# Performance work log

Hardware: AMD Instinct MI355X
Metric: run time of the kernel (lower is better)

Reference implementation:

```python
import jax, jax.numpy as jnp
import numpy as np
import math

B, S, D, H = 2, 2048, 1024, 16
HD = D // H  # 64 head dim
DFF = 4 * D
ROPE_BASE = 10000.0
EPS = 1e-5


def setup_inputs() -> dict:
    key = jax.random.key(0)
    ks = jax.random.split(key, 16)
    w = lambda k, shp: jax.random.normal(k, shp, jnp.float32) * 0.02
    return {
        "x": jax.random.normal(ks[0], (B, S, D), jnp.float32),
        "Wq": w(ks[1], (D, D)), "bq": jnp.zeros((D,), jnp.float32),
        "Wk": w(ks[2], (D, D)), "bk": jnp.zeros((D,), jnp.float32),
        "Wv": w(ks[3], (D, D)), "bv": jnp.zeros((D,), jnp.float32),
        "Wo": w(ks[4], (D, D)), "bo": jnp.zeros((D,), jnp.float32),
        "W1": w(ks[5], (D, DFF)), "b1": jnp.zeros((DFF,), jnp.float32),
        "W2": w(ks[6], (DFF, D)), "b2": jnp.zeros((D,), jnp.float32),
        "g_pre": jnp.ones((D,), jnp.float32), "be_pre": jnp.zeros((D,), jnp.float32),
        "g_post": jnp.ones((D,), jnp.float32), "be_post": jnp.zeros((D,), jnp.float32),
    }


def _layernorm(x, g, b):
    mu = jnp.mean(x, axis=-1, keepdims=True)
    var = jnp.mean(jnp.square(x - mu), axis=-1, keepdims=True)
    return (x - mu) * jax.lax.rsqrt(var + EPS) * g + b


def _rope(q, k):
    # q,k: [B,H,S,HD]; standard rotary embedding on head dim
    half = HD // 2
    inv_freq = 1.0 / (ROPE_BASE ** (jnp.arange(0, HD, 2, dtype=jnp.float32) / HD))  # [half]
    pos = jnp.arange(S, dtype=jnp.float32)
    freqs = pos[:, None] * inv_freq[None, :]           # [S, half]
    emb = jnp.concatenate([freqs, freqs], axis=-1)      # [S, HD]
    cos = jnp.cos(emb)[None, None]                      # [1,1,S,HD]
    sin = jnp.sin(emb)[None, None]

    def rot_half(t):
        return jnp.concatenate([-t[..., half:], t[..., :half]], axis=-1)

    return q * cos + rot_half(q) * sin, k * cos + rot_half(k) * sin


def reference(x, Wq, bq, Wk, bk, Wv, bv, Wo, bo, W1, b1, W2, b2,
              g_pre, be_pre, g_post, be_post):
    residual = x
    xn = _layernorm(x, g_pre, be_pre)

    def split_heads(t):  # [B,S,D] -> [B,H,S,HD]
        return t.reshape(B, S, H, HD).transpose(0, 2, 1, 3)

    q = split_heads(xn @ Wq + bq)
    k = split_heads(xn @ Wk + bk)
    v = split_heads(xn @ Wv + bv)
    q, k = _rope(q, k)

    scores = jnp.einsum("bhqd,bhkd->bhqk", q, k) / math.sqrt(HD)
    attn = jax.nn.softmax(scores, axis=-1)
    # NOTE: original applies causal mask AFTER softmax with fill -1e9 (no renorm)
    causal = jnp.tril(jnp.ones((S, S), jnp.float32))
    attn = jnp.where(causal == 0, jnp.float32(-1e9), attn)

    out = jnp.einsum("bhqk,bhkd->bhqd", attn, v)        # [B,H,S,HD]
    out = out.transpose(0, 2, 1, 3).reshape(B, S, D)
    out = out @ Wo + bo
    x = residual + out

    residual = x
    xn = _layernorm(x, g_post, be_post)
    ff = jax.nn.relu(xn @ W1 + b1) @ W2 + b2
    return residual + ff
```

## Files before the change

kernel.cpp:

```cpp
#include <hip/hip_runtime.h>
#include <stdint.h>

#define B_ 2
#define S_ 2048
#define D_ 1024
#define H_ 16
#define HD_ 64
#define DFF_ 4096
#define M_ 4096
#define QKV_STR 3072

typedef float           f4_t  __attribute__((ext_vector_type(4)));
typedef unsigned int    ui4_t __attribute__((ext_vector_type(4)));
typedef unsigned int    ui2_t __attribute__((ext_vector_type(2)));
typedef unsigned short  us4_t __attribute__((ext_vector_type(4)));
typedef unsigned short  us8_t __attribute__((ext_vector_type(8)));
typedef __bf16          bf8_t __attribute__((ext_vector_type(8)));

__device__ __forceinline__ float b2f(unsigned short u) {
    union { unsigned int u; float f; } v; v.u = ((unsigned int)u) << 16; return v.f;
}
__device__ __forceinline__ unsigned short f2b(float f) {
    union { float f; unsigned int u; } v; v.f = f;
    unsigned int u = v.u + 0x7fffu + ((v.u >> 16) & 1u);
    return (unsigned short)(u >> 16);
}
__device__ __forceinline__ unsigned cvt_pk_bf16(float lo, float hi) {
    unsigned r;
    asm("v_cvt_pk_bf16_f32 %0, %1, %2" : "=v"(r) : "v"(lo), "v"(hi));
    return r;
}
__device__ __forceinline__ void gll16(const unsigned short* g, unsigned short* l) {
    __builtin_amdgcn_global_load_lds((const __attribute__((address_space(1))) unsigned int*)g,
                                     (__attribute__((address_space(3))) unsigned int*)l,
                                     16, 0, 0);
}

__global__ __launch_bounds__(256) void k_transpose(const float* __restrict__ in,
                                                   unsigned short* __restrict__ out,
                                                   int R, int C) {
    __shared__ float tile[32][33];
    const int bc = blockIdx.x * 32, br = blockIdx.y * 32;
    const int tx = threadIdx.x & 31, ty = threadIdx.x >> 5;
#pragma unroll
    for (int i = ty; i < 32; i += 8)
        tile[i][tx] = in[(size_t)(br + i) * C + bc + tx];
    __syncthreads();
#pragma unroll
    for (int i = ty; i < 32; i += 8)
        out[(size_t)(bc + i) * R + br + tx] = f2b(tile[tx][i]);
}

__global__ __launch_bounds__(256) void k_bias3(const float* __restrict__ a,
                                               const float* __restrict__ b,
                                               const float* __restrict__ c,
                                               float* __restrict__ o) {
    const int t = blockIdx.x * 256 + threadIdx.x;
    if (t < 1024) o[t] = a[t];
    else if (t < 2048) o[t] = b[t - 1024];
    else o[t] = c[t - 2048];
}

__global__ __launch_bounds__(256) void k_layernorm(const float* __restrict__ x,
                                                   const float* __restrict__ g,
                                                   const float* __restrict__ be,
                                                   unsigned short* __restrict__ out) {
    const int row = blockIdx.x;
    const int t = threadIdx.x;
    const float* xr = x + (size_t)row * D_;
    f4_t v = *(const f4_t*)&xr[t * 4];
    float s = v[0] + v[1] + v[2] + v[3];
#pragma unroll
    for (int o = 32; o >= 1; o >>= 1) s += __shfl_down(s, o);
    __shared__ float red[4];
    const int w = t >> 6, lane = t & 63;
    if (lane == 0) red[w] = s;
    __syncthreads();
    const float mean = (red[0] + red[1] + red[2] + red[3]) * (1.f / D_);
    f4_t d;
#pragma unroll
    for (int c = 0; c < 4; c++) d[c] = v[c] - mean;
    float ss = d[0]*d[0] + d[1]*d[1] + d[2]*d[2] + d[3]*d[3];
#pragma unroll
    for (int o = 32; o >= 1; o >>= 1) ss += __shfl_down(ss, o);
    __syncthreads();
    if (lane == 0) red[w] = ss;
    __syncthreads();
    const float var = (red[0] + red[1] + red[2] + red[3]) * (1.f / D_);
    const float rstd = rsqrtf(var + 1e-5f);
    f4_t gv = *(const f4_t*)&g[t * 4];
    f4_t bv = *(const f4_t*)&be[t * 4];
    us4_t o4;
#pragma unroll
    for (int c = 0; c < 4; c++) o4[c] = f2b(d[c] * rstd * gv[c] + bv[c]);
    *(us4_t*)&out[(size_t)row * D_ + t * 4] = o4;
}

template<int RELU, int BF16OUT, int RESID>
__global__ __launch_bounds__(256) void k_gemm_bt(const unsigned short* __restrict__ A,
                                                 const unsigned short* __restrict__ Bt,
                                                 const float* __restrict__ bias,
                                                 const float* __restrict__ resid,
                                                 void* __restrict__ Cout,
                                                 int M, int N, int K) {
    __shared__ __align__(16) unsigned short As0[128 * 32];
    __shared__ __align__(16) unsigned short Bs0[128 * 32];
    __shared__ __align__(16) unsigned short As1[128 * 32];
    __shared__ __align__(16) unsigned short Bs1[128 * 32];
    const int tid = threadIdx.x;
    const int m0 = blockIdx.y * 128, n0 = blockIdx.x * 128;
    const int w = tid >> 6, lane = tid & 63;
    const int wr = w >> 1, wc = w & 1;
    const int lr = lane & 15, lg = lane >> 4;

    f4_t acc[4][4] = {};

    const int r1 = tid >> 2, q1 = tid & 3;
    const unsigned short* pA1 = A + (size_t)(m0 + r1) * K + q1 * 8;
    const unsigned short* pA2 = pA1 + (size_t)64 * K;
    const unsigned short* pB1 = Bt + (size_t)(n0 + r1) * K + q1 * 8;
    const unsigned short* pB2 = pB1 + (size_t)64 * K;
    const int wofs = w * 512;

#define STAGE(AS, BS, kk) do {                 \
        gll16(pA1 + (kk), (AS) + wofs);        \
        gll16(pA2 + (kk), (AS) + 2048 + wofs); \
        gll16(pB1 + (kk), (BS) + wofs);        \
        gll16(pB2 + (kk), (BS) + 2048 + wofs); } while (0)

#define COMPUTE(AS, BS) do {                                                     \
        bf8_t af[4], bfr[4];                                                     \
        _Pragma("unroll")                                                        \
        for (int f = 0; f < 4; f++) {                                            \
            af[f]  = *(const bf8_t*)&(AS)[(wr * 64 + f * 16 + lr) * 32 + lg * 8];\
            bfr[f] = *(const bf8_t*)&(BS)[(wc * 64 + f * 16 + lr) * 32 + lg * 8];\
        }                                                                        \
        _Pragma("unroll")                                                        \
        for (int mf = 0; mf < 4; mf++)                                           \
            _Pragma("unroll")                                                    \
            for (int nf = 0; nf < 4; nf++)                                       \
                acc[mf][nf] = __builtin_amdgcn_mfma_f32_16x16x32_bf16(           \
                    af[mf], bfr[nf], acc[mf][nf], 0, 0, 0); } while (0)

    STAGE(As0, Bs0, 0);
    for (int k0 = 0; k0 + 64 < K; k0 += 64) {
        STAGE(As1, Bs1, k0 + 32);
        asm volatile("s_waitcnt vmcnt(4)" ::: "memory");
        __builtin_amdgcn_s_barrier();
        COMPUTE(As0, Bs0);
        __builtin_amdgcn_s_barrier();
        STAGE(As0, Bs0, k0 + 64);
        asm volatile("s_waitcnt vmcnt(4)" ::: "memory");
        __builtin_amdgcn_s_barrier();
        COMPUTE(As1, Bs1);
        __builtin_amdgcn_s_barrier();
    }
    STAGE(As1, Bs1, K - 32);
    asm volatile("s_waitcnt vmcnt(4)" ::: "memory");
    __builtin_amdgcn_s_barrier();
    COMPUTE(As0, Bs0);
    asm volatile("s_waitcnt vmcnt(0)" ::: "memory");
    __builtin_amdgcn_s_barrier();
    COMPUTE(As1, Bs1);
#undef STAGE
#undef COMPUTE

#pragma unroll
    for (int mf = 0; mf < 4; mf++) {
#pragma unroll
        for (int nf = 0; nf < 4; nf++) {
            const int n = n0 + wc * 64 + nf * 16 + lr;
            const float bv = bias[n];
#pragma unroll
            for (int j = 0; j < 4; j++) {
                const int m = m0 + wr * 64 + mf * 16 + lg * 4 + j;
                float val = acc[mf][nf][j] + bv;
                if (RESID) val += resid[(size_t)m * N + n];
                if (RELU) val = fmaxf(val, 0.f);
                if (BF16OUT) ((unsigned short*)Cout)[(size_t)m * N + n] = f2b(val);
                else         ((float*)Cout)[(size_t)m * N + n] = val;
            }
        }
    }
}

template<int RELU, int BF16OUT, int RESID>
__global__ __launch_bounds__(256) void k_gemm64(const unsigned short* __restrict__ A,
                                                const unsigned short* __restrict__ Bt,
                                                const float* __restrict__ bias,
                                                const float* __restrict__ resid,
                                                void* __restrict__ Cout,
                                                int M, int N, int K) {
    __shared__ __align__(16) unsigned short As0[64 * 32];
    __shared__ __align__(16) unsigned short Bs0[128 * 32];
    __shared__ __align__(16) unsigned short As1[64 * 32];
    __shared__ __align__(16) unsigned short Bs1[128 * 32];
    const int tid = threadIdx.x;
    const int m0 = blockIdx.y * 64, n0 = blockIdx.x * 128;
    const int w = tid >> 6, lane = tid & 63;
    const int wr = w >> 1, wc = w & 1;
    const int lr = lane & 15, lg = lane >> 4;

    f4_t acc[2][4] = {};

    const int r1 = tid >> 2, q1 = tid & 3;
    const unsigned short* pA1 = A + (size_t)(m0 + r1) * K + q1 * 8;
    const unsigned short* pB1 = Bt + (size_t)(n0 + r1) * K + q1 * 8;
    const unsigned short* pB2 = pB1 + (size_t)64 * K;
    const int wofs = w * 512;

#define STAGE(AS, BS, kk) do {                 \
        gll16(pA1 + (kk), (AS) + wofs);        \
        gll16(pB1 + (kk), (BS) + wofs);        \
        gll16(pB2 + (kk), (BS) + 2048 + wofs); } while (0)

#define COMPUTE(AS, BS) do {                                                     \
        bf8_t af[2], bfr[4];                                                     \
        _Pragma("unroll")                                                        \
        for (int f = 0; f < 2; f++)                                              \
            af[f] = *(const bf8_t*)&(AS)[(wr * 32 + f * 16 + lr) * 32 + lg * 8]; \
        _Pragma("unroll")                                                        \
        for (int f = 0; f < 4; f++)                                              \
            bfr[f] = *(const bf8_t*)&(BS)[(wc * 64 + f * 16 + lr) * 32 + lg * 8];\
        _Pragma("unroll")                                                        \
        for (int mf = 0; mf < 2; mf++)                                           \
            _Pragma("unroll")                                                    \
            for (int nf = 0; nf < 4; nf++)                                       \
                acc[mf][nf] = __builtin_amdgcn_mfma_f32_16x16x32_bf16(           \
                    af[mf], bfr[nf], acc[mf][nf], 0, 0, 0); } while (0)

    STAGE(As0, Bs0, 0);
    for (int k0 = 0; k0 + 64 < K; k0 += 64) {
        STAGE(As1, Bs1, k0 + 32);
        asm volatile("s_waitcnt vmcnt(3)" ::: "memory");
        __builtin_amdgcn_s_barrier();
        COMPUTE(As0, Bs0);
        __builtin_amdgcn_s_barrier();
        STAGE(As0, Bs0, k0 + 64);
        asm volatile("s_waitcnt vmcnt(3)" ::: "memory");
        __builtin_amdgcn_s_barrier();
        COMPUTE(As1, Bs1);
        __builtin_amdgcn_s_barrier();
    }
    STAGE(As1, Bs1, K - 32);
    asm volatile("s_waitcnt vmcnt(3)" ::: "memory");
    __builtin_amdgcn_s_barrier();
    COMPUTE(As0, Bs0);
    asm volatile("s_waitcnt vmcnt(0)" ::: "memory");
    __builtin_amdgcn_s_barrier();
    COMPUTE(As1, Bs1);
#undef STAGE
#undef COMPUTE

#pragma unroll
    for (int mf = 0; mf < 2; mf++) {
#pragma unroll
        for (int nf = 0; nf < 4; nf++) {
            const int n = n0 + wc * 64 + nf * 16 + lr;
            const float bv = bias[n];
#pragma unroll
            for (int j = 0; j < 4; j++) {
                const int m = m0 + wr * 32 + mf * 16 + lg * 4 + j;
                float val = acc[mf][nf][j] + bv;
                if (RESID) val += resid[(size_t)m * N + n];
                if (RELU) val = fmaxf(val, 0.f);
                if (BF16OUT) ((unsigned short*)Cout)[(size_t)m * N + n] = f2b(val);
                else         ((float*)Cout)[(size_t)m * N + n] = val;
            }
        }
    }
}

__global__ __launch_bounds__(256) void k_rope(unsigned short* __restrict__ QKV) {
    const int idx = blockIdx.x * 256 + threadIdx.x;
    const int i = idx & 31;
    const int h = (idx >> 5) & 15;
    const int s = (idx >> 9) & 2047;
    const int b = idx >> 20;
    const float freq = exp2f(-(float)i * 0.4152410118609203f);
    const float ang = (float)s * freq;
    float sn, cs;
    sincosf(ang, &sn, &cs);
    const size_t base = ((size_t)(b * S_ + s)) * QKV_STR + h * HD_ + i;
    {
        float a = b2f(QKV[base]), c2 = b2f(QKV[base + 32]);
        QKV[base]      = f2b(a * cs - c2 * sn);
        QKV[base + 32] = f2b(c2 * cs + a * sn);
    }
    {
        float a = b2f(QKV[base + 1024]), c2 = b2f(QKV[base + 1024 + 32]);
        QKV[base + 1024]      = f2b(a * cs - c2 * sn);
        QKV[base + 1024 + 32] = f2b(c2 * cs + a * sn);
    }
}

__global__ __launch_bounds__(256) void k_vchunksum(const unsigned short* __restrict__ V,
                                                   float* __restrict__ sums) {
    const int blk = blockIdx.x;
    const int bh = blk >> 5, c = blk & 31;
    const int b = bh >> 4, h = bh & 15;
    const int d = threadIdx.x & 63, r4 = threadIdx.x >> 6;
    const unsigned short* base = V + ((size_t)(b * S_ + c * 64 + r4 * 16)) * QKV_STR + h * HD_ + d;
    float s = 0.f;
#pragma unroll
    for (int r = 0; r < 16; r++) s += b2f(base[(size_t)r * QKV_STR]);
    __shared__ float red[4][64];
    red[r4][d] = s;
    __syncthreads();
    if (r4 == 0) sums[(size_t)blk * 64 + d] = red[0][d] + red[1][d] + red[2][d] + red[3][d];
}

__global__ __launch_bounds__(64) void k_vscan(const float* __restrict__ sums,
                                              float* __restrict__ pre) {
    const int bh = blockIdx.x, d = threadIdx.x;
    float cum = 0.f;
    for (int c = 0; c < 32; c++) {
        pre[((size_t)bh * 33 + c) * 64 + d] = cum;
        cum += sums[((size_t)bh * 32 + c) * 64 + d];
    }
    pre[((size_t)bh * 33 + 32) * 64 + d] = cum;
}

#define KS_STRIDE 72

__global__ __launch_bounds__(256) void k_attn_mfma(const unsigned short* __restrict__ QKV,
                                                   const float* __restrict__ vpre,
                                                   unsigned short* __restrict__ Out) {
    __shared__ __align__(16) unsigned short Ks[2][64 * KS_STRIDE];
    __shared__ __align__(16) unsigned short Vt[2][64 * 64];
    __shared__ __align__(16) unsigned short Ps[4][2][16 * KS_STRIDE];

    const int id = blockIdx.x;
    const int wg = (id & 7) * 64 + (id >> 3);
    const int qblk = 15 - (wg & 15);
    const int bh = wg >> 4;
    const int b = bh >> 4, h = bh & 15;
    const int q0 = qblk * 128;
    const int tid = threadIdx.x;
    const int wq = tid >> 6;
    const int lane = tid & 63;
    const int lr = lane & 15, lg = lane >> 4;

    const unsigned short* Qp = QKV;
    const unsigned short* Kp = QKV + 1024;
    const unsigned short* Vp = QKV + 2048;

    const int kcd = 2 * qblk + (wq >> 1);
    const int lastV = 2 * qblk + 1;
    int qb[2];
    qb[0] = (wq & 1) * 32 + lr;
    qb[1] = qb[0] + 16;

    bf8_t qfrag[2][2];
#pragma unroll
    for (int t = 0; t < 2; t++) {
        const float qs = 0.125f * 1.44269504f;
        const size_t qbase = ((size_t)(b * S_ + q0 + wq * 32 + t * 16 + lr)) * QKV_STR + h * HD_;
#pragma unroll
        for (int ks = 0; ks < 2; ks++) {
            us8_t raw = *(const us8_t*)(Qp + qbase + ks * 32 + lg * 8);
            ui4_t p;
#pragma unroll
            for (int e = 0; e < 4; e++)
                p[e] = cvt_pk_bf16(b2f(raw[e * 2]) * qs, b2f(raw[e * 2 + 1]) * qs);
            union { ui4_t u; bf8_t b; } c; c.u = p;
            qfrag[t][ks] = c.b;
        }
    }

    const int row0 = tid >> 3, g = tid & 7;
    const int row1 = row0 + 32;
    const int r7 = row0 & 7;
    const int wv = tid >> 6;
    const unsigned short* pK0 = Kp + ((size_t)(b * S_ + row0)) * QKV_STR + h * HD_ + g * 8;
    const unsigned short* pK1 = Kp + ((size_t)(b * S_ + row1)) * QKV_STR + h * HD_ + g * 8;
    const unsigned short* pV0 = Vp + ((size_t)(b * S_ + row0)) * QKV_STR + h * HD_ + g * 8;
    const unsigned short* pV1 = Vp + ((size_t)(b * S_ + row1)) * QKV_STR + h * HD_ + g * 8;
    const int sw0 = (wv ^ g) << 3;
    const int sw1 = ((wv + 4) ^ g) << 3;

    float l_run[2] = {0.f, 0.f};
    f4_t acc_o[2][4] = {};
    f4_t acc_pre[2][4] = {};

    ui4_t ck0 = *(const ui4_t*)pK0;
    ui4_t ck1 = *(const ui4_t*)pK1;
    ui4_t cv0 = *(const ui4_t*)pV0;
    ui4_t cv1 = *(const ui4_t*)pV1;
    *(ui4_t*)&Ks[0][row0 * KS_STRIDE + g * 8] = ck0;
    *(ui4_t*)&Ks[0][row1 * KS_STRIDE + g * 8] = ck1;
    {
        const unsigned short* v0 = (const unsigned short*)&cv0;
        const unsigned short* v1 = (const unsigned short*)&cv1;
#pragma unroll
        for (int e = 0; e < 8; e++) {
            const int d = g * 8 + e;
            Vt[0][d * 64 + sw0 + r7] = v0[e];
            Vt[0][d * 64 + sw1 + r7] = v1[e];
        }
    }
    {
        const size_t koff = (size_t)64 * QKV_STR;
        ck0 = *(const ui4_t*)(pK0 + koff);
        ck1 = *(const ui4_t*)(pK1 + koff);
        cv0 = *(const ui4_t*)(pV0 + koff);
        cv1 = *(const ui4_t*)(pV1 + koff);
    }
    __syncthreads();

    for (int kc = 0; kc < 32; kc++) {
        const int cur = kc & 1;
        const unsigned short* Kc = Ks[cur];
        const unsigned short* Vc = Vt[cur];

        f4_t s4[2][4] = {};
        __builtin_amdgcn_s_setprio(1);
#pragma unroll
        for (int ks = 0; ks < 2; ks++) {
#pragma unroll
            for (int kk = 0; kk < 4; kk++) {
                bf8_t kfr = *(const bf8_t*)&Kc[(kk * 16 + lr) * KS_STRIDE + ks * 32 + lg * 8];
                s4[0][kk] = __builtin_amdgcn_mfma_f32_16x16x32_bf16(kfr, qfrag[0][ks], s4[0][kk], 0, 0, 0);
                s4[1][kk] = __builtin_amdgcn_mfma_f32_16x16x32_bf16(kfr, qfrag[1][ks], s4[1][kk], 0, 0, 0);
            }
        }
        __builtin_amdgcn_s_setprio(0);

        if (kc < 31) {
            unsigned short* Kn = Ks[cur ^ 1];
            *(ui4_t*)&Kn[row0 * KS_STRIDE + g * 8] = ck0;
            *(ui4_t*)&Kn[row1 * KS_STRIDE + g * 8] = ck1;
            if (kc + 1 <= lastV) {
                unsigned short* Vn = Vt[cur ^ 1];
                const unsigned short* v0 = (const unsigned short*)&cv0;
                const unsigned short* v1 = (const unsigned short*)&cv1;
#pragma unroll
                for (int e = 0; e < 8; e++) {
                    const int d = g * 8 + e;
                    Vn[d * 64 + sw0 + r7] = v0[e];
                    Vn[d * 64 + sw1 + r7] = v1[e];
                }
            }
        }
        if (kc < 30) {
            const size_t koff = (size_t)(kc + 2) * 64 * QKV_STR;
            ck0 = *(const ui4_t*)(pK0 + koff);
            ck1 = *(const ui4_t*)(pK1 + koff);
            if (kc + 2 <= lastV) {
                cv0 = *(const ui4_t*)(pV0 + koff);
                cv1 = *(const ui4_t*)(pV1 + koff);
            }
        }

#pragma unroll
        for (int t = 0; t < 2; t++) {
            float cs = 0.f;
#pragma unroll
            for (int kk = 0; kk < 4; kk++)
#pragma unroll
                for (int j = 0; j < 4; j++) {
                    const float p = __builtin_amdgcn_exp2f(s4[t][kk][j]);
                    s4[t][kk][j] = p;
                    cs += p;
                }
            cs += __shfl_xor(cs, 16);
            cs += __shfl_xor(cs, 32);
            l_run[t] += cs;
        }

        if (kc <= kcd) {
#pragma unroll
            for (int t = 0; t < 2; t++) {
                unsigned short* Pw = Ps[wq][t];
#pragma unroll
                for (int kk = 0; kk < 4; kk++) {
                    const int kb = kk * 16 + lg * 4;
                    ui2_t wd;
                    if (kc == kcd) {
                        wd[0] = cvt_pk_bf16(kb + 0 <= qb[t] ? s4[t][kk][0] : 0.f,
                                            kb + 1 <= qb[t] ? s4[t][kk][1] : 0.f);
                        wd[1] = cvt_pk_bf16(kb + 2 <= qb[t] ? s4[t][kk][2] : 0.f,
                                            kb + 3 <= qb[t] ? s4[t][kk][3] : 0.f);
                    } else {
                        wd[0] = cvt_pk_bf16(s4[t][kk][0], s4[t][kk][1]);
                        wd[1] = cvt_pk_bf16(s4[t][kk][2], s4[t][kk][3]);
                    }
                    *(ui2_t*)&Pw[lr * KS_STRIDE + kk * 16 + lg * 4] = wd;
                }
            }
            __builtin_amdgcn_s_setprio(1);
#pragma unroll
            for (int ks = 0; ks < 2; ks++) {
                bf8_t pf0 = *(const bf8_t*)&Ps[wq][0][lr * KS_STRIDE + ks * 32 + lg * 8];
                bf8_t pf1 = *(const bf8_t*)&Ps[wq][1][lr * KS_STRIDE + ks * 32 + lg * 8];
#pragma unroll
                for (int dd = 0; dd < 4; dd++) {
                    bf8_t vf = *(const bf8_t*)&Vc[(dd * 16 + lr) * 64 +
                                                  (((ks * 4 + lg) ^ ((dd * 2 + (lr >> 3)) & 7)) << 3)];
                    acc_o[0][dd] = __builtin_amdgcn_mfma_f32_16x16x32_bf16(vf, pf0, acc_o[0][dd], 0, 0, 0);
                    acc_o[1][dd] = __builtin_amdgcn_mfma_f32_16x16x32_bf16(vf, pf1, acc_o[1][dd], 0, 0, 0);
                }
            }
            __builtin_amdgcn_s_setprio(0);

            if (kc == kcd) {
#pragma unroll
                for (int t = 0; t < 2; t++) {
                    unsigned short* Pw = Ps[wq][t];
#pragma unroll
                    for (int kk = 0; kk < 4; kk++) {
                        const int kb = kk * 16 + lg * 4;
                        ui2_t wd;
                        wd[0] = (kb + 0 <= qb[t] ? 0x3f80u : 0u) | ((kb + 1 <= qb[t] ? 0x3f80u : 0u) << 16);
                        wd[1] = (kb + 2 <= qb[t] ? 0x3f80u : 0u) | ((kb + 3 <= qb[t] ? 0x3f80u : 0u) << 16);
                        *(ui2_t*)&Pw[lr * KS_STRIDE + kk * 16 + lg * 4] = wd;
                    }
                }
#pragma unroll
                for (int ks = 0; ks < 2; ks++) {
                    bf8_t pf0 = *(const bf8_t*)&Ps[wq][0][lr * KS_STRIDE + ks * 32 + lg * 8];
                    bf8_t pf1 = *(const bf8_t*)&Ps[wq][1][lr * KS_STRIDE + ks * 32 + lg * 8];
#pragma unroll
                    for (int dd = 0; dd < 4; dd++) {
                        bf8_t vf = *(const bf8_t*)&Vc[(dd * 16 + lr) * 64 +
                                                      (((ks * 4 + lg) ^ ((dd * 2 + (lr >> 3)) & 7)) << 3)];
                        acc_pre[0][dd] = __builtin_amdgcn_mfma_f32_16x16x32_bf16(vf, pf0, acc_pre[0][dd], 0, 0, 0);
                        acc_pre[1][dd] = __builtin_amdgcn_mfma_f32_16x16x32_bf16(vf, pf1, acc_pre[1][dd], 0, 0, 0);
                    }
                }
            }
        }
        __syncthreads();
    }

    const float* Cq = vpre + ((size_t)bh * 33 + kcd) * 64;
    const float* Ct = vpre + ((size_t)bh * 33 + 32) * 64;
#pragma unroll
    for (int t = 0; t < 2; t++) {
        const float inv_l = 1.f / l_run[t];
        const size_t obase = ((size_t)(b * S_ + q0 + wq * 32 + t * 16 + lr)) * D_ + h * HD_;
#pragma unroll
        for (int dd = 0; dd < 4; dd++) {
            const f4_t tq4 = *(const f4_t*)&Cq[dd * 16 + lg * 4];
            const f4_t tt4 = *(const f4_t*)&Ct[dd * 16 + lg * 4];
            float v[4];
#pragma unroll
            for (int j = 0; j < 4; j++)
                v[j] = acc_o[t][dd][j] * inv_l - 1e9f * (tt4[j] - tq4[j] - acc_pre[t][dd][j]);
            ui2_t wd;
            wd[0] = cvt_pk_bf16(v[0], v[1]);
            wd[1] = cvt_pk_bf16(v[2], v[3]);
            *(ui2_t*)&Out[obase + dd * 16 + lg * 4] = wd;
        }
    }
}

extern "C" void kernel_launch(void* const* d_in, const int* in_sizes, int n_in,
                              void* d_out, int out_size, void* d_ws, size_t ws_size,
                              hipStream_t stream) {
    const float* x     = (const float*)d_in[0];
    const float* Wq    = (const float*)d_in[1];  const float* bq = (const float*)d_in[2];
    const float* Wk    = (const float*)d_in[3];  const float* bk = (const float*)d_in[4];
    const float* Wv    = (const float*)d_in[5];  const float* bv = (const float*)d_in[6];
    const float* Wo    = (const float*)d_in[7];  const float* bo = (const float*)d_in[8];
    const float* W1    = (const float*)d_in[9];  const float* b1 = (const float*)d_in[10];
    const float* W2    = (const float*)d_in[11]; const float* b2 = (const float*)d_in[12];
    const float* gpre  = (const float*)d_in[13]; const float* bepre  = (const float*)d_in[14];
    const float* gpost = (const float*)d_in[15]; const float* bepost = (const float*)d_in[16];

    char* ws = (char*)d_ws;
    const size_t MB = 1024 * 1024;
    unsigned short* WqkvT = (unsigned short*)(ws + 0 * MB);
    unsigned short* WoT   = (unsigned short*)(ws + 6 * MB);
    unsigned short* W1T   = (unsigned short*)(ws + 8 * MB);
    unsigned short* W2T   = (unsigned short*)(ws + 16 * MB);
    unsigned short* xn    = (unsigned short*)(ws + 24 * MB);
    unsigned short* QKV   = (unsigned short*)(ws + 32 * MB);
    unsigned short* att   = (unsigned short*)(ws + 56 * MB);
    unsigned short* h1    = (unsigned short*)(ws + 24 * MB);
    unsigned short* x2n   = (unsigned short*)(ws + 56 * MB);
    float*          x2    = (float*)(ws + 64 * MB);
    float*          bqkv  = (float*)(ws + 80 * MB);
    float*          vpre  = (float*)(ws + 80 * MB + 16384);
    float*          vsum  = (float*)(ws + 81 * MB);

    k_transpose<<<dim3(32, 32),  256, 0, stream>>>(Wq, WqkvT, D_, D_);
    k_transpose<<<dim3(32, 32),  256, 0, stream>>>(Wk, WqkvT + 1024 * 1024, D_, D_);
    k_transpose<<<dim3(32, 32),  256, 0, stream>>>(Wv, WqkvT + 2048 * 1024, D_, D_);
    k_transpose<<<dim3(32, 32),  256, 0, stream>>>(Wo, WoT, D_, D_);
    k_transpose<<<dim3(128, 32), 256, 0, stream>>>(W1, W1T, D_, DFF_);
    k_transpose<<<dim3(32, 128), 256, 0, stream>>>(W2, W2T, DFF_, D_);
    k_bias3<<<12, 256, 0, stream>>>(bq, bk, bv, bqkv);

    k_layernorm<<<M_, 256, 0, stream>>>(x, gpre, bepre, xn);

    k_gemm_bt<0, 1, 0><<<dim3(24, 32), 256, 0, stream>>>(xn, WqkvT, bqkv, nullptr, QKV, M_, QKV_STR, D_);

    k_rope<<<8192, 256, 0, stream>>>(QKV);
    k_vchunksum<<<1024, 256, 0, stream>>>(QKV + 2048, vsum);
    k_vscan<<<32, 64, 0, stream>>>(vsum, vpre);

    k_attn_mfma<<<512, 256, 0, stream>>>(QKV, vpre, att);

    k_gemm64<0, 0, 1><<<dim3(8, 64), 256, 0, stream>>>(att, WoT, bo, x, x2, M_, D_, D_);

    k_layernorm<<<M_, 256, 0, stream>>>(x2, gpost, bepost, x2n);

    k_gemm_bt<1, 1, 0><<<dim3(32, 32), 256, 0, stream>>>(x2n, W1T, b1, nullptr, h1, M_, DFF_, D_);
    k_gemm64<0, 0, 1><<<dim3(8, 64), 256, 0, stream>>>(h1, W2T, b2, x2, (float*)d_out, M_, D_, DFF_);
}
```

Measured before the change: 268.1 us.

## Deepen GEMM LDS pipeline to four stages and reswizzle attention V tile

Both GEMM kernels go from a double-buffered LDS pipeline to a four-buffer ring. Global-to-LDS loads are issued two k-steps ahead, and the trailing barrier after each compute is removed, so memory latency overlaps more with MFMA work. The attention kernel's transposed V layout gains an extra XOR term on the element index, to cut LDS bank conflicts on the scalar transposed stores, and the read swizzle is changed to match. The cost is doubled LDS per GEMM block, which may reduce occupancy. Dropping the post-compute barrier depends on the ring depth to avoid write-after-read hazards.

```diff
diff --git a/kernel.cpp b/kernel.cpp
--- a/kernel.cpp
+++ b/kernel.cpp
@@ -95,6 +95,9 @@
     for (int c = 0; c < 4; c++) o4[c] = f2b(d[c] * rstd * gv[c] + bv[c]);
     *(us4_t*)&out[(size_t)row * D_ + t * 4] = o4;
 }
+
+#define VMW(n) asm volatile("s_waitcnt vmcnt(" #n ")" ::: "memory")
+#define BAR()  __builtin_amdgcn_s_barrier()
 
 template<int RELU, int BF16OUT, int RESID>
 __global__ __launch_bounds__(256) void k_gemm_bt(const unsigned short* __restrict__ A,
@@ -107,6 +110,10 @@
     __shared__ __align__(16) unsigned short Bs0[128 * 32];
     __shared__ __align__(16) unsigned short As1[128 * 32];
     __shared__ __align__(16) unsigned short Bs1[128 * 32];
+    __shared__ __align__(16) unsigned short As2[128 * 32];
+    __shared__ __align__(16) unsigned short Bs2[128 * 32];
+    __shared__ __align__(16) unsigned short As3[128 * 32];
+    __shared__ __align__(16) unsigned short Bs3[128 * 32];
     const int tid = threadIdx.x;
     const int m0 = blockIdx.y * 128, n0 = blockIdx.x * 128;
     const int w = tid >> 6, lane = tid & 63;
@@ -143,25 +150,18 @@
                     af[mf], bfr[nf], acc[mf][nf], 0, 0, 0); } while (0)
 
     STAGE(As0, Bs0, 0);
-    for (int k0 = 0; k0 + 64 < K; k0 += 64) {
-        STAGE(As1, Bs1, k0 + 32);
-        asm volatile("s_waitcnt vmcnt(4)" ::: "memory");
-        __builtin_amdgcn_s_barrier();
-        COMPUTE(As0, Bs0);
-        __builtin_amdgcn_s_barrier();
-        STAGE(As0, Bs0, k0 + 64);
-        asm volatile("s_waitcnt vmcnt(4)" ::: "memory");
-        __builtin_amdgcn_s_barrier();
-        COMPUTE(As1, Bs1);
-        __builtin_amdgcn_s_barrier();
-    }
-    STAGE(As1, Bs1, K - 32);
-    asm volatile("s_waitcnt vmcnt(4)" ::: "memory");
-    __builtin_amdgcn_s_barrier();
-    COMPUTE(As0, Bs0);
-    asm volatile("s_waitcnt vmcnt(0)" ::: "memory");
-    __builtin_amdgcn_s_barrier();
-    COMPUTE(As1, Bs1);
+    STAGE(As1, Bs1, 32);
+    int k0 = 0;
+    for (; k0 + 256 <= K; k0 += 128) {
+        STAGE(As2, Bs2, k0 + 64);  VMW(8); BAR(); COMPUTE(As0, Bs0);
+        STAGE(As3, Bs3, k0 + 96);  VMW(8); BAR(); COMPUTE(As1, Bs1);
+        STAGE(As0, Bs0, k0 + 128); VMW(8); BAR(); COMPUTE(As2, Bs2);
+        STAGE(As1, Bs1, k0 + 160); VMW(8); BAR(); COMPUTE(As3, Bs3);
+    }
+    STAGE(As2, Bs2, K - 64); VMW(8); BAR(); COMPUTE(As0, Bs0);
+    STAGE(As3, Bs3, K - 32); VMW(8); BAR(); COMPUTE(As1, Bs1);
+    VMW(4); BAR(); COMPUTE(As2, Bs2);
+    VMW(0); BAR(); COMPUTE(As3, Bs3);
 #undef STAGE
 #undef COMPUTE
 
@@ -195,6 +195,10 @@
     __shared__ __align__(16) unsigned short Bs0[128 * 32];
     __shared__ __align__(16) unsigned short As1[64 * 32];
     __shared__ __align__(16) unsigned short Bs1[128 * 32];
+    __shared__ __align__(16) unsigned short As2[64 * 32];
+    __shared__ __align__(16) unsigned short Bs2[128 * 32];
+    __shared__ __align__(16) unsigned short As3[64 * 32];
+    __shared__ __align__(16) unsigned short Bs3[128 * 32];
     const int tid = threadIdx.x;
     const int m0 = blockIdx.y * 64, n0 = blockIdx.x * 128;
     const int w = tid >> 6, lane = tid & 63;
@@ -230,25 +234,18 @@
                     af[mf], bfr[nf], acc[mf][nf], 0, 0, 0); } while (0)
 
     STAGE(As0, Bs0, 0);
-    for (int k0 = 0; k0 + 64 < K; k0 += 64) {
-        STAGE(As1, Bs1, k0 + 32);
-        asm volatile("s_waitcnt vmcnt(3)" ::: "memory");
-        __builtin_amdgcn_s_barrier();
-        COMPUTE(As0, Bs0);
-        __builtin_amdgcn_s_barrier();
-        STAGE(As0, Bs0, k0 + 64);
-        asm volatile("s_waitcnt vmcnt(3)" ::: "memory");
-        __builtin_amdgcn_s_barrier();
-        COMPUTE(As1, Bs1);
-        __builtin_amdgcn_s_barrier();
-    }
-    STAGE(As1, Bs1, K - 32);
-    asm volatile("s_waitcnt vmcnt(3)" ::: "memory");
-    __builtin_amdgcn_s_barrier();
-    COMPUTE(As0, Bs0);
-    asm volatile("s_waitcnt vmcnt(0)" ::: "memory");
-    __builtin_amdgcn_s_barrier();
-    COMPUTE(As1, Bs1);
+    STAGE(As1, Bs1, 32);
+    int k0 = 0;
+    for (; k0 + 256 <= K; k0 += 128) {
+        STAGE(As2, Bs2, k0 + 64);  VMW(6); BAR(); COMPUTE(As0, Bs0);
+        STAGE(As3, Bs3, k0 + 96);  VMW(6); BAR(); COMPUTE(As1, Bs1);
+        STAGE(As0, Bs0, k0 + 128); VMW(6); BAR(); COMPUTE(As2, Bs2);
+        STAGE(As1, Bs1, k0 + 160); VMW(6); BAR(); COMPUTE(As3, Bs3);
+    }
+    STAGE(As2, Bs2, K - 64); VMW(6); BAR(); COMPUTE(As0, Bs0);
+    STAGE(As3, Bs3, K - 32); VMW(6); BAR(); COMPUTE(As1, Bs1);
+    VMW(3); BAR(); COMPUTE(As2, Bs2);
+    VMW(0); BAR(); COMPUTE(As3, Bs3);
 #undef STAGE
 #undef COMPUTE
 
@@ -376,8 +373,6 @@
     const unsigned short* pK1 = Kp + ((size_t)(b * S_ + row1)) * QKV_STR + h * HD_ + g * 8;
     const unsigned short* pV0 = Vp + ((size_t)(b * S_ + row0)) * QKV_STR + h * HD_ + g * 8;
     const unsigned short* pV1 = Vp + ((size_t)(b * S_ + row1)) * QKV_STR + h * HD_ + g * 8;
-    const int sw0 = (wv ^ g) << 3;
-    const int sw1 = ((wv + 4) ^ g) << 3;
 
     float l_run[2] = {0.f, 0.f};
     f4_t acc_o[2][4] = {};
@@ -395,8 +390,8 @@
 #pragma unroll
         for (int e = 0; e < 8; e++) {
             const int d = g * 8 + e;
-            Vt[0][d * 64 + sw0 + r7] = v0[e];
-            Vt[0][d * 64 + sw1 + r7] = v1[e];
+            Vt[0][d * 64 + ((wv ^ g ^ e) << 3) + r7] = v0[e];
+            Vt[0][d * 64 + (((wv + 4) ^ g ^ e) << 3) + r7] = v1[e];
         }
     }
     {
@@ -407,6 +402,8 @@
         cv1 = *(const ui4_t*)(pV1 + koff);
     }
     __syncthreads();
+
+#define VSLOT(dd, ks) ((((ks) * 4 + lg) ^ (lr & 7) ^ (((dd) * 2 + (lr >> 3)) & 7)) << 3)
 
     for (int kc = 0; kc < 32; kc++) {
         const int cur = kc & 1;
@@ -437,8 +434,8 @@
 #pragma unroll
                 for (int e = 0; e < 8; e++) {
                     const int d = g * 8 + e;
-                    Vn[d * 64 + sw0 + r7] = v0[e];
-                    Vn[d * 64 + sw1 + r7] = v1[e];
+                    Vn[d * 64 + ((wv ^ g ^ e) << 3) + r7] = v0[e];
+                    Vn[d * 64 + (((wv + 4) ^ g ^ e) << 3) + r7] = v1[e];
                 }
             }
         }
@@ -495,8 +492,7 @@
                 bf8_t pf1 = *(const bf8_t*)&Ps[wq][1][lr * KS_STRIDE + ks * 32 + lg * 8];
 #pragma unroll
                 for (int dd = 0; dd < 4; dd++) {
-                    bf8_t vf = *(const bf8_t*)&Vc[(dd * 16 + lr) * 64 +
-                                                  (((ks * 4 + lg) ^ ((dd * 2 + (lr >> 3)) & 7)) << 3)];
+                    bf8_t vf = *(const bf8_t*)&Vc[(dd * 16 + lr) * 64 + VSLOT(dd, ks)];
                     acc_o[0][dd] = __builtin_amdgcn_mfma_f32_16x16x32_bf16(vf, pf0, acc_o[0][dd], 0, 0, 0);
                     acc_o[1][dd] = __builtin_amdgcn_mfma_f32_16x16x32_bf16(vf, pf1, acc_o[1][dd], 0, 0, 0);
                 }
@@ -522,8 +518,7 @@
                     bf8_t pf1 = *(const bf8_t*)&Ps[wq][1][lr * KS_STRIDE + ks * 32 + lg * 8];
 #pragma unroll
                     for (int dd = 0; dd < 4; dd++) {
-                        bf8_t vf = *(const bf8_t*)&Vc[(dd * 16 + lr) * 64 +
-                                                      (((ks * 4 + lg) ^ ((dd * 2 + (lr >> 3)) & 7)) << 3)];
+                        bf8_t vf = *(const bf8_t*)&Vc[(dd * 16 + lr) * 64 + VSLOT(dd, ks)];
                         acc_pre[0][dd] = __builtin_amdgcn_mfma_f32_16x16x32_bf16(vf, pf0, acc_pre[0][dd], 0, 0, 0);
                         acc_pre[1][dd] = __builtin_amdgcn_mfma_f32_16x16x32_bf16(vf, pf1, acc_pre[1][dd], 0, 0, 0);
                     }
@@ -532,6 +527,7 @@
         }
         __syncthreads();
     }
+#undef VSLOT
 
     const float* Cq = vpre + ((size_t)bh * 33 + kcd) * 64;
     const float* Ct = vpre + ((size_t)bh * 33 + 32) * 64;
```

Result: slower. 296.7 us (+10.7%).
